# Performance work log

Hardware: AMD Instinct MI355X
Metric: run time of the kernel (lower is better)

The kernel has to match this reference:

```python
import jax, jax.numpy as jnp
import numpy as np

S, B, CLS = 14, 2, 20
L_COORD, L_NOOBJ = 5.0, 0.5
BATCH = 8192
C = 5 * B + CLS  # 30


def setup_inputs() -> dict:
    key = jax.random.key(0)
    k1, k2, k3 = jax.random.split(key, 3)
    pred = jax.random.normal(k1, (BATCH, S, S, C), dtype=jnp.float32)
    target = jax.random.uniform(k2, (BATCH, S, S, C), dtype=jnp.float32)
    # replicate the conf bit into both box slots (channels 4 and 9)
    obj = (jax.random.uniform(k3, (BATCH, S, S)) > 0.9).astype(jnp.float32)
    target = target.at[..., 4].set(obj)
    target = target.at[..., 9].set(obj)
    return {"pred": pred, "target": target}


def _decode(box5):
    # box5: [..., 5] = (cx, cy, sqrt_w, sqrt_h, conf) -> corners [..., 4]
    x, y, sw, sh = box5[..., 0], box5[..., 1], box5[..., 2], box5[..., 3]
    hw = 0.5 * sw * sw
    hh = 0.5 * sh * sh
    return jnp.stack([x - hw, y - hh, x + hw, y + hh], axis=-1)


def _iou(b1, b2):
    # elementwise IoU over matching rows, like compute_iou with N==M paired rows
    lt = jnp.maximum(b1[..., :2], b2[..., :2])
    rb = jnp.minimum(b1[..., 2:], b2[..., 2:])
    wh = jnp.maximum(rb - lt, 0.0)
    inter = wh[..., 0] * wh[..., 1]
    a1 = (b1[..., 2] - b1[..., 0]) * (b1[..., 3] - b1[..., 1])
    a2 = (b2[..., 2] - b2[..., 0]) * (b2[..., 3] - b2[..., 1])
    denom = a1 + a2 - inter
    safe = jnp.where(denom > 0, denom, 1.0)
    return jnp.where(denom > 0, inter / safe, 0.0)


def reference(pred, target):
    batch = pred.shape[0]
    p = pred.reshape(-1, C)    # [N, 30], N = batch*S*S
    t = target.reshape(-1, C)
    objf = (t[:, 4] > 0).astype(p.dtype)   # [N]
    noobjf = 1.0 - objf

    p_boxes = p[:, :5 * B].reshape(-1, B, 5)   # [N, B, 5]
    t_boxes = t[:, :5 * B].reshape(-1, B, 5)

    iou = _iou(_decode(t_boxes), _decode(p_boxes))   # [N, B]
    max_iou = jnp.max(iou, axis=1)                   # [N]
    max_idx = jnp.argmax(iou, axis=1)                # [N]
    sel = jax.nn.one_hot(max_idx, B, dtype=p.dtype)  # [N, B] response mask
    p_sel = jnp.einsum('nb,nbk->nk', sel, p_boxes)   # [N, 5] responsible pred box
    t_sel = jnp.einsum('nb,nbk->nk', sel, t_boxes)

    # localization: xy + sqrt-wh MSE on responsible box, obj cells only
    local = jnp.sum(objf[:, None] * (p_sel[:, :4] - t_sel[:, :4]) ** 2)
    # classification MSE, obj cells only
    cls_loss = jnp.sum(objf[:, None] * (p[:, 5 * B:] - t[:, 5 * B:]) ** 2)
    # containment: pred conf of responsible box vs (detached) max IoU
    miou_sg = jax.lax.stop_gradient(max_iou)
    contain = jnp.sum(objf * (p_sel[:, 4] - miou_sg) ** 2)
    # no-object: conf of all B boxes in empty cells
    noobj = jnp.sum(noobjf[:, None] * (p_boxes[:, :, 4] - t_boxes[:, :, 4]) ** 2)
    # iou loss: detached max IoU vs target conf of responsible box
    iou_loss = jnp.sum(objf * (miou_sg - t_sel[:, 4]) ** 2)

    loss_all = (L_COORD * local + cls_loss + contain
                + L_NOOBJ * noobj + iou_loss) / batch
    return loss_all
```

## Files before the change

kernel.cpp:

```cpp
#include <hip/hip_runtime.h>

#define SS 14
#define NBOX 2
#define CCH 30
#define TILE_CELLS 64
#define TILE_FLOATS (TILE_CELLS * CCH)
#define WAVES_PER_BLOCK 4

typedef __attribute__((address_space(1))) const void as1_void;
typedef __attribute__((address_space(3))) void as3_void;

__device__ __forceinline__ void stage_tile(const float* __restrict__ g,
                                           float* l, int lane) {
    const char* gc = (const char*)g;
    char* lc = (char*)l;
#pragma unroll
    for (int j = 0; j < 7; ++j)
        __builtin_amdgcn_global_load_lds((as1_void*)(gc + j * 1024 + lane * 16),
                                         (as3_void*)(lc + j * 1024), 16, 0, 0);
#pragma unroll
    for (int j = 0; j < 2; ++j)
        __builtin_amdgcn_global_load_lds((as1_void*)(gc + 7168 + j * 256 + lane * 4),
                                         (as3_void*)(lc + 7168 + j * 256), 4, 0, 0);
}

__device__ __forceinline__ float cell_loss(const float* p, const float* t) {
    float iou0 = 0.f, iou1 = 0.f, loc0 = 0.f, loc1 = 0.f;
#pragma unroll
    for (int b = 0; b < NBOX; ++b) {
        const int o = 5 * b;
        float thw = 0.5f * t[o + 2] * t[o + 2];
        float thh = 0.5f * t[o + 3] * t[o + 3];
        float phw = 0.5f * p[o + 2] * p[o + 2];
        float phh = 0.5f * p[o + 3] * p[o + 3];
        float t0x = t[o + 0] - thw, t0y = t[o + 1] - thh;
        float t1x = t[o + 0] + thw, t1y = t[o + 1] + thh;
        float p0x = p[o + 0] - phw, p0y = p[o + 1] - phh;
        float p1x = p[o + 0] + phw, p1y = p[o + 1] + phh;

        float ltx = fmaxf(t0x, p0x), lty = fmaxf(t0y, p0y);
        float rbx = fminf(t1x, p1x), rby = fminf(t1y, p1y);
        float w = fmaxf(rbx - ltx, 0.0f);
        float h = fmaxf(rby - lty, 0.0f);
        float inter = w * h;
        float a1 = (t1x - t0x) * (t1y - t0y);
        float a2 = (p1x - p0x) * (p1y - p0y);
        float denom = a1 + a2 - inter;
        float iou_b = (denom > 0.0f) ? (inter / denom) : 0.0f;

        float l = 0.0f;
#pragma unroll
        for (int k = 0; k < 4; ++k) {
            float d = p[o + k] - t[o + k];
            l += d * d;
        }
        if (b == 0) { iou0 = iou_b; loc0 = l; }
        else        { iou1 = iou_b; loc1 = l; }
    }

    int sel1 = (iou1 > iou0);
    float max_iou = fmaxf(iou0, iou1);
    float loc   = sel1 ? loc1 : loc0;
    float pconf = sel1 ? p[9] : p[4];
    float tconf = sel1 ? t[9] : t[4];

    float cls = 0.0f;
#pragma unroll
    for (int k = 5 * NBOX; k < CCH; ++k) {
        float d = p[k] - t[k];
        cls += d * d;
    }

    float dcon = pconf - max_iou;
    float d4 = p[4] - t[4];
    float d9 = p[9] - t[9];
    float noobj = d4 * d4 + d9 * d9;
    float diou = max_iou - tconf;

    float objf = (t[4] > 0.0f) ? 1.0f : 0.0f;
    return objf * (5.0f * loc + cls + dcon * dcon + diou * diou)
         + (1.0f - objf) * 0.5f * noobj;
}

__global__ __launch_bounds__(256) void yolov1_loss_kernel(
    const float* __restrict__ pred, const float* __restrict__ target,
    float* __restrict__ out, int ncells, float inv_batch)
{
    __shared__ __align__(16) float lds[WAVES_PER_BLOCK * 2 * TILE_FLOATS];

    const int lane = threadIdx.x & 63;
    const int wid  = threadIdx.x >> 6;
    const int w    = blockIdx.x * WAVES_PER_BLOCK + wid;
    const int W    = gridDim.x * WAVES_PER_BLOCK;
    const int ntiles = ncells / TILE_CELLS;

    float* myp = lds + wid * (2 * TILE_FLOATS);
    float* myt = myp + TILE_FLOATS;

    float acc = 0.0f;
    int tile = w;
    if (tile < ntiles) {
        stage_tile(pred   + (size_t)tile * TILE_FLOATS, myp, lane);
        stage_tile(target + (size_t)tile * TILE_FLOATS, myt, lane);
        for (;;) {
            const int next = tile + W;
            asm volatile("s_waitcnt vmcnt(0)" ::: "memory");
            __builtin_amdgcn_sched_barrier(0);

            float p[CCH], t[CCH];
            const float2* pl = (const float2*)(myp + lane * CCH);
            const float2* tl = (const float2*)(myt + lane * CCH);
#pragma unroll
            for (int k = 0; k < CCH / 2; ++k) {
                float2 a = pl[k]; p[2 * k] = a.x; p[2 * k + 1] = a.y;
                float2 b = tl[k]; t[2 * k] = b.x; t[2 * k + 1] = b.y;
            }
            asm volatile("s_waitcnt lgkmcnt(0)" ::: "memory");
            __builtin_amdgcn_sched_barrier(0);

            if (next < ntiles) {
                stage_tile(pred   + (size_t)next * TILE_FLOATS, myp, lane);
                stage_tile(target + (size_t)next * TILE_FLOATS, myt, lane);
            }
            acc += cell_loss(p, t);
            if (next >= ntiles) break;
            tile = next;
        }
    }

    for (int cell = ntiles * TILE_CELLS + w * 64 + lane; cell < ncells;
         cell += W * 64) {
        float p[CCH], t[CCH];
        const float2* pp = (const float2*)(pred + (size_t)cell * CCH);
        const float2* tp = (const float2*)(target + (size_t)cell * CCH);
#pragma unroll
        for (int k = 0; k < CCH / 2; ++k) {
            float2 a = pp[k]; p[2 * k] = a.x; p[2 * k + 1] = a.y;
            float2 b = tp[k]; t[2 * k] = b.x; t[2 * k + 1] = b.y;
        }
        acc += cell_loss(p, t);
    }

#pragma unroll
    for (int off = 32; off > 0; off >>= 1)
        acc += __shfl_down(acc, off, 64);
    if (lane == 0)
        atomicAdd(out, acc * inv_batch);
}

extern "C" void kernel_launch(void* const* d_in, const int* in_sizes, int n_in,
                              void* d_out, int out_size, void* d_ws, size_t ws_size,
                              hipStream_t stream) {
    const float* pred = (const float*)d_in[0];
    const float* target = (const float*)d_in[1];
    float* out = (float*)d_out;

    int ncells = in_sizes[0] / CCH;
    int batch = ncells / (SS * SS);
    float inv_batch = 1.0f / (float)batch;

    hipMemsetAsync(d_out, 0, sizeof(float) * out_size, stream);

    const int threads = 256;
    int blocks = 512;
    yolov1_loss_kernel<<<blocks, threads, 0, stream>>>(pred, target, out,
                                                       ncells, inv_batch);
}
```

Baseline: 82.77 us.

## Double-buffer per-wave LDS tiles to keep two tile loads in flight

Each wave now owns two LDS buffer pairs. It prefetches tile t+2W while computing tile t, and waits with vmcnt(18) so the next tile's loads can stay outstanding. To fit the doubled LDS per wave, blocks shrink to 2 waves (128 threads) with the same 512 blocks, which halves the total wave count. Memory-level parallelism per wave goes up, but fewer waves are resident overall.

```diff
diff --git a/kernel.cpp b/kernel.cpp
--- a/kernel.cpp
+++ b/kernel.cpp
@@ -5,7 +5,8 @@
 #define CCH 30
 #define TILE_CELLS 64
 #define TILE_FLOATS (TILE_CELLS * CCH)
-#define WAVES_PER_BLOCK 4
+#define WAVES_PER_BLOCK 2
+#define OPS_PER_TILE 18
 
 typedef __attribute__((address_space(1))) const void as1_void;
 typedef __attribute__((address_space(3))) void as3_void;
@@ -82,11 +83,11 @@
          + (1.0f - objf) * 0.5f * noobj;
 }
 
-__global__ __launch_bounds__(256) void yolov1_loss_kernel(
+__global__ __launch_bounds__(128) void yolov1_loss_kernel(
     const float* __restrict__ pred, const float* __restrict__ target,
     float* __restrict__ out, int ncells, float inv_batch)
 {
-    __shared__ __align__(16) float lds[WAVES_PER_BLOCK * 2 * TILE_FLOATS];
+    __shared__ __align__(16) float lds[WAVES_PER_BLOCK * 4 * TILE_FLOATS];
 
     const int lane = threadIdx.x & 63;
     const int wid  = threadIdx.x >> 6;
@@ -94,22 +95,32 @@
     const int W    = gridDim.x * WAVES_PER_BLOCK;
     const int ntiles = ncells / TILE_CELLS;
 
-    float* myp = lds + wid * (2 * TILE_FLOATS);
-    float* myt = myp + TILE_FLOATS;
+    float* base = lds + wid * (4 * TILE_FLOATS);
+    float* curp = base;
+    float* curt = base + TILE_FLOATS;
+    float* nxtp = base + 2 * TILE_FLOATS;
+    float* nxtt = base + 3 * TILE_FLOATS;
 
     float acc = 0.0f;
-    int tile = w;
-    if (tile < ntiles) {
-        stage_tile(pred   + (size_t)tile * TILE_FLOATS, myp, lane);
-        stage_tile(target + (size_t)tile * TILE_FLOATS, myt, lane);
+    int t_cur = w;
+    if (t_cur < ntiles) {
+        stage_tile(pred   + (size_t)t_cur * TILE_FLOATS, curp, lane);
+        stage_tile(target + (size_t)t_cur * TILE_FLOATS, curt, lane);
+        if (t_cur + W < ntiles) {
+            stage_tile(pred   + (size_t)(t_cur + W) * TILE_FLOATS, nxtp, lane);
+            stage_tile(target + (size_t)(t_cur + W) * TILE_FLOATS, nxtt, lane);
+        }
         for (;;) {
-            const int next = tile + W;
-            asm volatile("s_waitcnt vmcnt(0)" ::: "memory");
+            const int t_pre = t_cur + 2 * W;
+            if (t_cur + W < ntiles)
+                asm volatile("s_waitcnt vmcnt(18)" ::: "memory");
+            else
+                asm volatile("s_waitcnt vmcnt(0)" ::: "memory");
             __builtin_amdgcn_sched_barrier(0);
 
             float p[CCH], t[CCH];
-            const float2* pl = (const float2*)(myp + lane * CCH);
-            const float2* tl = (const float2*)(myt + lane * CCH);
+            const float2* pl = (const float2*)(curp + lane * CCH);
+            const float2* tl = (const float2*)(curt + lane * CCH);
 #pragma unroll
             for (int k = 0; k < CCH / 2; ++k) {
                 float2 a = pl[k]; p[2 * k] = a.x; p[2 * k + 1] = a.y;
@@ -118,13 +129,17 @@
             asm volatile("s_waitcnt lgkmcnt(0)" ::: "memory");
             __builtin_amdgcn_sched_barrier(0);
 
-            if (next < ntiles) {
-                stage_tile(pred   + (size_t)next * TILE_FLOATS, myp, lane);
-                stage_tile(target + (size_t)next * TILE_FLOATS, myt, lane);
+            if (t_pre < ntiles) {
+                stage_tile(pred   + (size_t)t_pre * TILE_FLOATS, curp, lane);
+                stage_tile(target + (size_t)t_pre * TILE_FLOATS, curt, lane);
             }
             acc += cell_loss(p, t);
-            if (next >= ntiles) break;
-            tile = next;
+
+            t_cur += W;
+            if (t_cur >= ntiles) break;
+            float* s;
+            s = curp; curp = nxtp; nxtp = s;
+            s = curt; curt = nxtt; nxtt = s;
         }
     }
 
@@ -161,7 +176,7 @@
 
     hipMemsetAsync(d_out, 0, sizeof(float) * out_size, stream);
 
-    const int threads = 256;
+    const int threads = 128;
     int blocks = 512;
     yolov1_loss_kernel<<<blocks, threads, 0, stream>>>(pred, target, out,
                                                        ncells, inv_batch);
```

Result: faster. 77.80 us (median of 2 runs) (-6.0%).

## Replace global-to-LDS direct loads with register double-buffered prefetch pipeline

Applied to the files above, without the earlier changes.

Drops the global_load_lds staging and instead loads each tile into VGPRs as float2 loads, using two register buffers so the next tile's loads are in flight while the current one is written to LDS and processed. A partial vmcnt wait lets the older batch of loads complete while the newer ones stay outstanding. Launch bounds gain a minimum of 2 blocks per CU. The cost is a large register footprint of 60 float2 buffers and an extra LDS write pass per tile, which may limit occupancy.

```diff
diff --git a/kernel.cpp b/kernel.cpp
--- a/kernel.cpp
+++ b/kernel.cpp
@@ -6,23 +6,7 @@
 #define TILE_CELLS 64
 #define TILE_FLOATS (TILE_CELLS * CCH)
 #define WAVES_PER_BLOCK 4
-
-typedef __attribute__((address_space(1))) const void as1_void;
-typedef __attribute__((address_space(3))) void as3_void;
-
-__device__ __forceinline__ void stage_tile(const float* __restrict__ g,
-                                           float* l, int lane) {
-    const char* gc = (const char*)g;
-    char* lc = (char*)l;
-#pragma unroll
-    for (int j = 0; j < 7; ++j)
-        __builtin_amdgcn_global_load_lds((as1_void*)(gc + j * 1024 + lane * 16),
-                                         (as3_void*)(lc + j * 1024), 16, 0, 0);
-#pragma unroll
-    for (int j = 0; j < 2; ++j)
-        __builtin_amdgcn_global_load_lds((as1_void*)(gc + 7168 + j * 256 + lane * 4),
-                                         (as3_void*)(lc + 7168 + j * 256), 4, 0, 0);
-}
+#define NLOAD 15
 
 __device__ __forceinline__ float cell_loss(const float* p, const float* t) {
     float iou0 = 0.f, iou1 = 0.f, loc0 = 0.f, loc1 = 0.f;
@@ -82,7 +66,14 @@
          + (1.0f - objf) * 0.5f * noobj;
 }
 
-__global__ __launch_bounds__(256) void yolov1_loss_kernel(
+#define WAIT_VM30 do { asm volatile("s_waitcnt vmcnt(30)" ::: "memory"); \
+                       __builtin_amdgcn_sched_barrier(0); } while (0)
+#define WAIT_VM0  do { asm volatile("s_waitcnt vmcnt(0)" ::: "memory"); \
+                       __builtin_amdgcn_sched_barrier(0); } while (0)
+#define WAIT_LGKM0 do { asm volatile("s_waitcnt lgkmcnt(0)" ::: "memory"); \
+                        __builtin_amdgcn_sched_barrier(0); } while (0)
+
+__global__ __launch_bounds__(256, 2) void yolov1_loss_kernel(
     const float* __restrict__ pred, const float* __restrict__ target,
     float* __restrict__ out, int ncells, float inv_batch)
 {
@@ -97,34 +88,59 @@
     float* myp = lds + wid * (2 * TILE_FLOATS);
     float* myt = myp + TILE_FLOATS;
 
+#define ISSUE(RP, RT, TI) do {                                              \
+    const float2* gp = (const float2*)pred  + (size_t)(TI) * (TILE_FLOATS/2);\
+    const float2* gt = (const float2*)target + (size_t)(TI) * (TILE_FLOATS/2);\
+    _Pragma("unroll")                                                        \
+    for (int j = 0; j < NLOAD; ++j) {                                        \
+        RP[j] = gp[j * 64 + lane];                                           \
+        RT[j] = gt[j * 64 + lane];                                           \
+    } } while (0)
+
+#define WRITE_LDS(RP, RT) do {                                               \
+    _Pragma("unroll")                                                        \
+    for (int j = 0; j < NLOAD; ++j) {                                        \
+        *(float2*)(myp + j * 128 + lane * 2) = RP[j];                        \
+        *(float2*)(myt + j * 128 + lane * 2) = RT[j];                        \
+    } } while (0)
+
+#define PROCESS() do {                                                       \
+    float p[CCH], t[CCH];                                                    \
+    const float2* pl = (const float2*)(myp + lane * CCH);                    \
+    const float2* tl = (const float2*)(myt + lane * CCH);                    \
+    _Pragma("unroll")                                                        \
+    for (int k = 0; k < CCH / 2; ++k) {                                      \
+        float2 a = pl[k]; p[2 * k] = a.x; p[2 * k + 1] = a.y;                \
+        float2 b = tl[k]; t[2 * k] = b.x; t[2 * k + 1] = b.y;                \
+    }                                                                        \
+    acc += cell_loss(p, t); } while (0)
+
+    float2 rAp[NLOAD], rAt[NLOAD], rBp[NLOAD], rBt[NLOAD];
+
     float acc = 0.0f;
-    int tile = w;
-    if (tile < ntiles) {
-        stage_tile(pred   + (size_t)tile * TILE_FLOATS, myp, lane);
-        stage_tile(target + (size_t)tile * TILE_FLOATS, myt, lane);
+    int cur = w;
+    if (cur < ntiles) {
+        ISSUE(rAp, rAt, cur);
         for (;;) {
-            const int next = tile + W;
-            asm volatile("s_waitcnt vmcnt(0)" ::: "memory");
-            __builtin_amdgcn_sched_barrier(0);
+            int nxt = cur + W;
+            bool more = nxt < ntiles;
+            if (more) { ISSUE(rBp, rBt, nxt); WAIT_VM30; }
+            else      { WAIT_VM0; }
+            WRITE_LDS(rAp, rAt);
+            WAIT_LGKM0;
+            PROCESS();
+            if (!more) break;
+            cur = nxt;
 
-            float p[CCH], t[CCH];
-            const float2* pl = (const float2*)(myp + lane * CCH);
-            const float2* tl = (const float2*)(myt + lane * CCH);
-#pragma unroll
-            for (int k = 0; k < CCH / 2; ++k) {
-                float2 a = pl[k]; p[2 * k] = a.x; p[2 * k + 1] = a.y;
-                float2 b = tl[k]; t[2 * k] = b.x; t[2 * k + 1] = b.y;
-            }
-            asm volatile("s_waitcnt lgkmcnt(0)" ::: "memory");
-            __builtin_amdgcn_sched_barrier(0);
-
-            if (next < ntiles) {
-                stage_tile(pred   + (size_t)next * TILE_FLOATS, myp, lane);
-                stage_tile(target + (size_t)next * TILE_FLOATS, myt, lane);
-            }
-            acc += cell_loss(p, t);
-            if (next >= ntiles) break;
-            tile = next;
+            nxt = cur + W;
+            more = nxt < ntiles;
+            if (more) { ISSUE(rAp, rAt, nxt); WAIT_VM30; }
+            else      { WAIT_VM0; }
+            WRITE_LDS(rBp, rBt);
+            WAIT_LGKM0;
+            PROCESS();
+            if (!more) break;
+            cur = nxt;
         }
     }
 
```

Result: no change. 83.88 us (+1.3%).
